# Kernel optimization log

Measured on AMD Instinct MI355X. Metric: run time of the kernel, lower is better.

The kernel has to match this reference:

```python
import jax, jax.numpy as jnp
import numpy as np

DIM = 2048
H = 16
QLR = 1536
KVLR = 512
NOPE = 128
ROPE = 64
VH = 128
QKH = NOPE + ROPE  # 192
B, S = 2, 2048
EPS = 1e-6


def _rmsnorm(x, w):
    return x * jax.lax.rsqrt(jnp.mean(x * x, axis=-1, keepdims=True) + EPS) * w


def _rope_cos_sin(seq_len, r, dtype):
    inv_freq = 1.0 / (10000.0 ** (jnp.arange(0, r, 2, dtype=jnp.float32) / r))
    ang = jnp.arange(seq_len, dtype=jnp.float32)[:, None] * inv_freq  # [S, r/2]
    return jnp.cos(ang).astype(dtype), jnp.sin(ang).astype(dtype)


def _rot(t, cos, sin):
    # rotate-half RoPE on last dim; cos/sin pre-broadcast to t's rank
    t1, t2 = jnp.split(t, 2, axis=-1)
    return jnp.concatenate([t1 * cos - t2 * sin, t2 * cos + t1 * sin], axis=-1)


def setup_inputs() -> dict:
    key = jax.random.key(0)
    ks = jax.random.split(key, 12)
    sd = 0.02
    return {
        "x": jax.random.normal(ks[0], (B, S, DIM), jnp.float32),
        "wqd": jax.random.normal(ks[1], (DIM, QLR), jnp.float32) * sd,
        "bqd": jnp.zeros((QLR,), jnp.float32),
        "qnorm_w": jnp.ones((QLR,), jnp.float32),
        "wqu": jax.random.normal(ks[2], (QLR, H * QKH), jnp.float32) * sd,
        "bqu": jnp.zeros((H * QKH,), jnp.float32),
        "wkvd": jax.random.normal(ks[3], (DIM, KVLR + ROPE), jnp.float32) * sd,
        "bkvd": jnp.zeros((KVLR + ROPE,), jnp.float32),
        "kvnorm_w": jnp.ones((KVLR,), jnp.float32),
        "wkvu": jax.random.normal(ks[4], (KVLR, H * (NOPE + VH)), jnp.float32) * sd,
        "bkvu": jnp.zeros((H * (NOPE + VH),), jnp.float32),
        "wout": jax.random.normal(ks[5], (H * VH, DIM), jnp.float32) * sd,
        "bout": jnp.zeros((DIM,), jnp.float32),
    }


def reference(x, wqd, bqd, qnorm_w, wqu, bqu, wkvd, bkvd, kvnorm_w, wkvu, bkvu, wout, bout):
    b, s, _ = x.shape
    # Q path: low-rank down, RMSNorm, up; split nope / rope
    q = _rmsnorm(x @ wqd + bqd, qnorm_w) @ wqu + bqu        # [b,s,H*QKH]
    q = q.reshape(b, s, H, QKH)
    q_nope, q_rope = q[..., :NOPE], q[..., NOPE:]
    # KV path: joint down-proj -> kv latent + shared rope key
    kvd = x @ wkvd + bkvd                                   # [b,s,KVLR+ROPE]
    kv_lora, k_rope = kvd[..., :KVLR], kvd[..., KVLR:]
    cos, sin = _rope_cos_sin(s, ROPE, x.dtype)
    q_rope = _rot(q_rope, cos[None, :, None, :], sin[None, :, None, :])
    k_rope = _rot(k_rope, cos[None, :, :], sin[None, :, :])  # [b,s,ROPE]
    kvu = _rmsnorm(kv_lora, kvnorm_w) @ wkvu + bkvu          # [b,s,H*(NOPE+VH)]
    kvu = kvu.reshape(b, s, H, NOPE + VH)
    k_nope, v = kvu[..., :NOPE], kvu[..., NOPE:]
    k_rope_b = jnp.broadcast_to(k_rope[:, :, None, :], (b, s, H, ROPE))
    qf = jnp.concatenate([q_nope, q_rope], axis=-1)          # [b,s,H,QKH]
    kf = jnp.concatenate([k_nope, k_rope_b], axis=-1)        # [b,s,H,QKH]
    scale = QKH ** -0.5
    scores = jnp.einsum('bqhd,bkhd->bhqk', qf, kf) * scale
    causal = jnp.tril(jnp.ones((s, s), bool))
    scores = jnp.where(causal, scores, jnp.finfo(scores.dtype).min)
    attn = jax.nn.softmax(scores, axis=-1)
    o = jnp.einsum('bhqk,bkhd->bqhd', attn, v).reshape(b, s, H * VH)
    return o @ wout + bout
```

## Files before the change

### kernel.cpp

```cpp
#include <hip/hip_runtime.h>
#include <hip/hip_bf16.h>
#include <math.h>

#define HH 16
#define SS 2048
#define BBATCH 2
#define NROWS 4096

typedef __attribute__((ext_vector_type(8))) __bf16 bf16x8;
typedef __attribute__((ext_vector_type(4))) float f32x4;
typedef const __attribute__((address_space(1))) unsigned int* gas1_t;
typedef __attribute__((address_space(3))) unsigned int* las3_t;

__device__ __forceinline__ unsigned short f2bf(float f) {
  unsigned u = __builtin_bit_cast(unsigned, f);
  u += 0x7fffu + ((u >> 16) & 1u);
  return (unsigned short)(u >> 16);
}
__device__ __forceinline__ float bf2f(unsigned short u) {
  return __builtin_bit_cast(float, (unsigned)u << 16);
}

__device__ __forceinline__ void gload16(const void* g, void* l) {
  __builtin_amdgcn_global_load_lds((gas1_t)g, (las3_t)l, 16, 0, 0);
}
__device__ __forceinline__ f32x4 mfma16(bf16x8 a, bf16x8 b, f32x4 c) {
  return __builtin_amdgcn_mfma_f32_16x16x32_bf16(a, b, c, 0, 0, 0);
}

__device__ __forceinline__ void transpose_body(const float* __restrict__ W,
                                               unsigned short* __restrict__ Wt,
                                               int K, int N, int Npad,
                                               int bx, int by, float (*tile)[33], int tid) {
  int n0 = bx * 32, k0 = by * 32;
  int tx = tid & 31, ty = tid >> 5;
  for (int i = ty; i < 32; i += 8) {
    int k = k0 + i, n = n0 + tx;
    tile[i][tx] = (k < K && n < N) ? W[(long)k * N + n] : 0.f;
  }
  __syncthreads();
  for (int i = ty; i < 32; i += 8) {
    int n = n0 + i, k = k0 + tx;
    if (n < Npad && k < K) Wt[(long)n * K + k] = f2bf(tile[tx][i]);
  }
}

__global__ __launch_bounds__(256) void k_prep(const float* __restrict__ x,
                                              unsigned short* __restrict__ xb,
                                              const float* __restrict__ wqd,
                                              const float* __restrict__ wqu,
                                              const float* __restrict__ wkvd,
                                              const float* __restrict__ wkvu,
                                              const float* __restrict__ wout,
                                              unsigned short* __restrict__ wqkt,
                                              unsigned short* __restrict__ wqut,
                                              unsigned short* __restrict__ wkvut,
                                              unsigned short* __restrict__ woutt,
                                              const float* __restrict__ bqd,
                                              const float* __restrict__ bkvd,
                                              float* __restrict__ mbias,
                                              float2* __restrict__ rtab) {
  __shared__ float tile[32][33];
  int blk = blockIdx.x;
  int tid = threadIdx.x;
  if (blk < 2048) {
    long n4 = (long)NROWS * 2048 / 4;
    for (long i = (long)blk * 256 + tid; i < n4; i += 2048 * 256) {
      float4 v = ((const float4*)x)[i];
      ushort4 o = { f2bf(v.x), f2bf(v.y), f2bf(v.z), f2bf(v.w) };
      ((ushort4*)xb)[i] = o;
    }
  } else if (blk < 5120) {
    int t = blk - 2048;
    transpose_body(wqd, wqkt, 2048, 1536, 1536, t % 48, t / 48, tile, tid);
  } else if (blk < 9728) {
    int t = blk - 5120;
    transpose_body(wqu, wqut, 1536, 3072, 3072, t % 96, t / 96, tile, tid);
  } else if (blk < 11008) {
    int t = blk - 9728;
    transpose_body(wkvd, wqkt + (size_t)1536 * 2048, 2048, 576, 640, t % 20, t / 20, tile, tid);
  } else if (blk < 13056) {
    int t = blk - 11008;
    transpose_body(wkvu, wkvut, 512, 4096, 4096, t % 128, t / 128, tile, tid);
  } else if (blk < 17152) {
    int t = blk - 13056;
    transpose_body(wout, woutt, 2048, 2048, 2048, t % 64, t / 64, tile, tid);
  } else if (blk < 17161) {
    int i = (blk - 17152) * 256 + tid;
    if (i < 2176) mbias[i] = i < 1536 ? bqd[i] : (i < 2112 ? bkvd[i - 1536] : 0.f);
  } else {
    int t = blk - 17161;
    int s = t * 8 + (tid >> 5);
    int i = tid & 31;
    float inv = powf(10000.f, -(float)i / 32.f);
    float ang = (float)s * inv;
    float sn, cs;
    sincosf(ang, &sn, &cs);
    rtab[s * 32 + i] = make_float2(cs, sn);
  }
}

__global__ __launch_bounds__(256) void k_gemm(const unsigned short* __restrict__ A,
                                              const unsigned short* __restrict__ Bt,
                                              const float* __restrict__ bias,
                                              float* __restrict__ C,
                                              int M, int N, int K) {
  __shared__ unsigned short lA[128 * 32];
  __shared__ unsigned short lB[128 * 32];
  int tid = threadIdx.x;
  int wave = tid >> 6, lane = tid & 63;
  int l15 = lane & 15, lhi = lane >> 4;
  int ntn = (N + 127) >> 7;
  int tm = blockIdx.x / ntn, tn = blockIdx.x % ntn;
  long row0 = (long)tm * 128, col0 = (long)tn * 128;
  int wr = wave >> 1, wc = wave & 1;

  const unsigned short* gA = A + (row0 + (tid >> 2)) * K + (tid & 3) * 8;
  const unsigned short* gB = Bt + (col0 + (tid >> 2)) * K + (tid & 3) * 8;
  unsigned short* lA0 = &lA[tid * 8];
  unsigned short* lB0 = &lB[tid * 8];

  f32x4 acc[4][4] = {};
  for (int k0 = 0; k0 < K; k0 += 32) {
    __syncthreads();
    gload16(gA + k0, lA0);
    gload16(gA + (long)64 * K + k0, lA0 + 2048);
    gload16(gB + k0, lB0);
    gload16(gB + (long)64 * K + k0, lB0 + 2048);
    asm volatile("s_waitcnt vmcnt(0)" ::: "memory");
    __syncthreads();
    bf16x8 af[4], bfr[4];
#pragma unroll
    for (int i = 0; i < 4; ++i) {
      af[i]  = *(const bf16x8*)&lA[(wr * 64 + i * 16 + l15) * 32 + lhi * 8];
      bfr[i] = *(const bf16x8*)&lB[(wc * 64 + i * 16 + l15) * 32 + lhi * 8];
    }
#pragma unroll
    for (int i = 0; i < 4; ++i)
#pragma unroll
      for (int j = 0; j < 4; ++j)
        acc[i][j] = mfma16(af[i], bfr[j], acc[i][j]);
  }
#pragma unroll
  for (int i = 0; i < 4; ++i)
#pragma unroll
    for (int j = 0; j < 4; ++j) {
      long r = row0 + wr * 64 + i * 16 + lhi * 4;
      long c = col0 + wc * 64 + j * 16 + l15;
      if (c < N) {
        float bv = bias[c];
#pragma unroll
        for (int rr = 0; rr < 4; ++rr)
          C[(r + rr) * N + c] = acc[i][j][rr] + bv;
      }
    }
}

__global__ __launch_bounds__(256) void k_gemm_c16(const unsigned short* __restrict__ A,
                                                  const unsigned short* __restrict__ Bt,
                                                  const float* __restrict__ bias,
                                                  unsigned short* __restrict__ C,
                                                  int M, int N, int K) {
  __shared__ unsigned short lA[128 * 32];
  __shared__ unsigned short lB[128 * 32];
  int tid = threadIdx.x;
  int wave = tid >> 6, lane = tid & 63;
  int l15 = lane & 15, lhi = lane >> 4;
  int ntn = (N + 127) >> 7;
  int tm = blockIdx.x / ntn, tn = blockIdx.x % ntn;
  long row0 = (long)tm * 128, col0 = (long)tn * 128;
  int wr = wave >> 1, wc = wave & 1;

  const unsigned short* gA = A + (row0 + (tid >> 2)) * K + (tid & 3) * 8;
  const unsigned short* gB = Bt + (col0 + (tid >> 2)) * K + (tid & 3) * 8;
  unsigned short* lA0 = &lA[tid * 8];
  unsigned short* lB0 = &lB[tid * 8];

  f32x4 acc[4][4] = {};
  for (int k0 = 0; k0 < K; k0 += 32) {
    __syncthreads();
    gload16(gA + k0, lA0);
    gload16(gA + (long)64 * K + k0, lA0 + 2048);
    gload16(gB + k0, lB0);
    gload16(gB + (long)64 * K + k0, lB0 + 2048);
    asm volatile("s_waitcnt vmcnt(0)" ::: "memory");
    __syncthreads();
    bf16x8 af[4], bfr[4];
#pragma unroll
    for (int i = 0; i < 4; ++i) {
      af[i]  = *(const bf16x8*)&lA[(wr * 64 + i * 16 + l15) * 32 + lhi * 8];
      bfr[i] = *(const bf16x8*)&lB[(wc * 64 + i * 16 + l15) * 32 + lhi * 8];
    }
#pragma unroll
    for (int i = 0; i < 4; ++i)
#pragma unroll
      for (int j = 0; j < 4; ++j)
        acc[i][j] = mfma16(af[i], bfr[j], acc[i][j]);
  }
#pragma unroll
  for (int i = 0; i < 4; ++i)
#pragma unroll
    for (int j = 0; j < 4; ++j) {
      long r = row0 + wr * 64 + i * 16 + lhi * 4;
      long c = col0 + wc * 64 + j * 16 + l15;
      if (c < N) {
        float bv = bias[c];
#pragma unroll
        for (int rr = 0; rr < 4; ++rr)
          C[(r + rr) * N + c] = f2bf(acc[i][j][rr] + bv);
      }
    }
}

__global__ __launch_bounds__(256) void k_up(const unsigned short* __restrict__ qn,
                                            const unsigned short* __restrict__ wqut,
                                            const float* __restrict__ bqu,
                                            const unsigned short* __restrict__ kvn,
                                            const unsigned short* __restrict__ wkvut,
                                            const float* __restrict__ bkvu,
                                            const unsigned short* __restrict__ sCb,
                                            const float2* __restrict__ rtab,
                                            unsigned short* __restrict__ qf,
                                            unsigned short* __restrict__ kf3,
                                            unsigned short* __restrict__ vt3) {
  __shared__ unsigned short smem[16384];
  unsigned short* lA = smem;
  unsigned short* lB = smem + 4096;
  int blk = blockIdx.x;
  int tid = threadIdx.x;
  int wave = tid >> 6, lane = tid & 63;
  int l15 = lane & 15, lhi = lane >> 4;
  int wr = wave >> 1, wc = wave & 1;

  if (blk < 768) {
    const int N = 3072, K = 1536;
    int tm = blk / 24, tn = blk % 24;
    long row0 = (long)tm * 128, col0 = (long)tn * 128;
    const unsigned short* gA = qn + (row0 + (tid >> 2)) * K + (tid & 3) * 8;
    const unsigned short* gB = wqut + (col0 + (tid >> 2)) * K + (tid & 3) * 8;
    unsigned short* lA0 = &lA[tid * 8];
    unsigned short* lB0 = &lB[tid * 8];
    f32x4 acc[4][4] = {};
    for (int k0 = 0; k0 < K; k0 += 32) {
      __syncthreads();
      gload16(gA + k0, lA0);
      gload16(gA + (long)64 * K + k0, lA0 + 2048);
      gload16(gB + k0, lB0);
      gload16(gB + (long)64 * K + k0, lB0 + 2048);
      asm volatile("s_waitcnt vmcnt(0)" ::: "memory");
      __syncthreads();
      bf16x8 af[4], bfr[4];
#pragma unroll
      for (int i = 0; i < 4; ++i) {
        af[i]  = *(const bf16x8*)&lA[(wr * 64 + i * 16 + l15) * 32 + lhi * 8];
        bfr[i] = *(const bf16x8*)&lB[(wc * 64 + i * 16 + l15) * 32 + lhi * 8];
      }
#pragma unroll
      for (int i = 0; i < 4; ++i)
#pragma unroll
        for (int j = 0; j < 4; ++j)
          acc[i][j] = mfma16(af[i], bfr[j], acc[i][j]);
    }
    const float scq = 0.07216878364870322f * 1.4426950408889634f;
    int base = (int)col0 + wc * 64;
    int h = base / 192;
    int m192 = base - h * 192;
    float bv[4];
#pragma unroll
    for (int j = 0; j < 4; ++j) bv[j] = bqu[base + j * 16 + l15];
#pragma unroll
    for (int i = 0; i < 4; ++i) {
#pragma unroll
      for (int rr = 0; rr < 4; ++rr) {
        long r = row0 + wr * 64 + i * 16 + lhi * 4 + rr;
        int s = (int)(r & 2047), b = (int)(r >> 11);
        unsigned short* dst = qf + (((long)(b * HH + h)) * SS + s) * 192;
        if (m192 < 128) {
#pragma unroll
          for (int j = 0; j < 4; ++j)
            dst[m192 + j * 16 + l15] = f2bf((acc[i][j][rr] + bv[j]) * scq);
        } else {
#pragma unroll
          for (int j = 0; j < 2; ++j) {
            int ifq = j * 16 + l15;
            float2 cs = rtab[s * 32 + ifq];
            float v1 = acc[i][j][rr] + bv[j];
            float v2 = acc[i][j + 2][rr] + bv[j + 2];
            dst[128 + ifq] = f2bf((v1 * cs.x - v2 * cs.y) * scq);
            dst[160 + ifq] = f2bf((v2 * cs.x + v1 * cs.y) * scq);
          }
        }
      }
    }
  } else if (blk < 1792) {
    const int N = 4096, K = 512;
    int b2 = blk - 768;
    int tm = b2 / 32, tn = b2 % 32;
    long row0 = (long)tm * 128, col0 = (long)tn * 128;
    const unsigned short* gA = kvn + (row0 + (tid >> 2)) * K + (tid & 3) * 8;
    const unsigned short* gB = wkvut + (col0 + (tid >> 2)) * K + (tid & 3) * 8;
    unsigned short* lA0 = &lA[tid * 8];
    unsigned short* lB0 = &lB[tid * 8];
    f32x4 acc[4][4] = {};
    for (int k0 = 0; k0 < K; k0 += 32) {
      __syncthreads();
      gload16(gA + k0, lA0);
      gload16(gA + (long)64 * K + k0, lA0 + 2048);
      gload16(gB + k0, lB0);
      gload16(gB + (long)64 * K + k0, lB0 + 2048);
      asm volatile("s_waitcnt vmcnt(0)" ::: "memory");
      __syncthreads();
      bf16x8 af[4], bfr[4];
#pragma unroll
      for (int i = 0; i < 4; ++i) {
        af[i]  = *(const bf16x8*)&lA[(wr * 64 + i * 16 + l15) * 32 + lhi * 8];
        bfr[i] = *(const bf16x8*)&lB[(wc * 64 + i * 16 + l15) * 32 + lhi * 8];
      }
#pragma unroll
      for (int i = 0; i < 4; ++i)
#pragma unroll
        for (int j = 0; j < 4; ++j)
          acc[i][j] = mfma16(af[i], bfr[j], acc[i][j]);
    }
    int base = (int)col0 + wc * 64;
    int h = base >> 8;
    bool isv = (base & 255) >= 128;
    float bv[4];
#pragma unroll
    for (int j = 0; j < 4; ++j) bv[j] = bkvu[base + j * 16 + l15];
    int b = (int)(row0 >> 11);
    long bh = (long)b * HH + h;
    int lrb = wr * 64;
    __syncthreads();
    if (isv) {
#pragma unroll
      for (int i = 0; i < 4; ++i) {
        int lr = lrb + i * 16 + lhi * 4;
#pragma unroll
        for (int j = 0; j < 4; ++j) {
          int lc = wc * 64 + j * 16 + l15;
          ushort4 pk = { f2bf(acc[i][j][0] + bv[j]), f2bf(acc[i][j][1] + bv[j]),
                         f2bf(acc[i][j][2] + bv[j]), f2bf(acc[i][j][3] + bv[j]) };
          *(ushort4*)&smem[((lr >> 5) << 12) + lc * 32 + (lr & 31)] = pk;
        }
      }
      __syncthreads();
      long dst0 = (bh * 64 + ((row0 & 2047) >> 5)) * 4096;
#pragma unroll
      for (int p = 0; p < 8; ++p) {
        int e = p * 256 + tid;
        *(uint4*)&vt3[dst0 + e * 8] = *(uint4*)&smem[e * 8];
      }
    } else {
#pragma unroll
      for (int i = 0; i < 4; ++i) {
        int lr0 = lrb + i * 16 + lhi * 4;
#pragma unroll
        for (int j = 0; j < 4; ++j) {
          int c = (base & 255) + j * 16 + l15;
          int tbase = ((lr0 >> 4) << 11) + ((c >> 5) << 9) + (((c >> 3) & 3) << 7) + (c & 7);
#pragma unroll
          for (int rr = 0; rr < 4; ++rr)
            smem[tbase + ((lr0 + rr) & 15) * 8] = f2bf(acc[i][j][rr] + bv[j]);
        }
      }
      __syncthreads();
      long kb3 = (bh * 128 + ((row0 & 2047) >> 4)) * 3072;
#pragma unroll
      for (int p = 0; p < 8; ++p) {
        int e = p * 256 + tid;
        int tile = e >> 6;
        int off = (e & 63) * 8;
        long dst = kb3 + ((long)(tile >> 2) * 6 + (tile & 3)) * 512 + off;
        *(uint4*)&kf3[dst] = *(uint4*)&smem[tile * 512 + off];
      }
    }
  } else {
    int t = blk - 1792;
    int bs = t * 4 + (tid >> 6);
    int s = bs & (SS - 1), b = bs >> 11;
    const unsigned short* src = sCb + (long)bs * 2176 + 2048;
    int i = lane & 31;
    float2 cs = rtab[s * 32 + i];
    float t1 = bf2f(src[i]), t2 = bf2f(src[32 + i]);
    float v = (lane < 32) ? (t1 * cs.x - t2 * cs.y) : (t2 * cs.x + t1 * cs.y);
    unsigned short bv = f2bf(v);
    int d = 128 + lane;
    long inner = (long)(d >> 5) * 512 + ((d >> 3) & 3) * 128 + (s & 15) * 8 + (d & 7);
#pragma unroll
    for (int h = 0; h < HH; ++h) {
      long kblk = ((long)(b * HH + h) * 128 + (s >> 4)) * 6;
      kf3[kblk * 512 + inner] = bv;
    }
  }
}

__global__ __launch_bounds__(256) void k_rmsnorm2(const unsigned short* __restrict__ sC,
                                                  const float* __restrict__ qnw,
                                                  const float* __restrict__ kvnw,
                                                  unsigned short* __restrict__ qn,
                                                  unsigned short* __restrict__ kvn) {
  int blk = blockIdx.x;
  long row;
  const unsigned short* x;
  const float* w;
  unsigned short* y;
  int L;
  if (blk < NROWS) {
    row = blk; x = sC + row * 2176; w = qnw; y = qn + row * 1536; L = 1536;
  } else {
    row = blk - NROWS; x = sC + row * 2176 + 1536; w = kvnw; y = kvn + row * 512; L = 512;
  }
  float ss = 0.f;
  int n4 = L >> 2;
  for (int i = threadIdx.x; i < n4; i += 256) {
    ushort4 v = ((const ushort4*)x)[i];
    float a = bf2f(v.x), bb = bf2f(v.y), c = bf2f(v.z), d = bf2f(v.w);
    ss += a * a + bb * bb + c * c + d * d;
  }
  for (int off = 32; off > 0; off >>= 1) ss += __shfl_xor(ss, off);
  __shared__ float sb[4];
  if ((threadIdx.x & 63) == 0) sb[threadIdx.x >> 6] = ss;
  __syncthreads();
  float scale = rsqrtf((sb[0] + sb[1] + sb[2] + sb[3]) / (float)L + 1e-6f);
  for (int i = threadIdx.x; i < L; i += 256)
    y[i] = f2bf(bf2f(x[i]) * scale * w[i]);
}

__global__ __launch_bounds__(256, 4) void k_attn(const unsigned short* __restrict__ qf,
                                                 const unsigned short* __restrict__ kf3,
                                                 const unsigned short* __restrict__ vt3,
                                                 unsigned short* __restrict__ o,
                                                 float* __restrict__ pO,
                                                 float* __restrict__ pml) {
  __shared__ unsigned short kbuf[64 * 192];
  __shared__ unsigned short pbuf[4][16 * 72];
  int tid = threadIdx.x;
  int wave = tid >> 6, lane = tid & 63;
  int l15 = lane & 15, lhi = lane >> 4;
  int idx = blockIdx.x;
  int rp = idx >> 5, bh = idx & 31;
  int qt, part, np;
  if (rp < 32)      { qt = 24 + (rp >> 2); part = rp & 3; np = 4; }
  else if (rp < 56) { int r = rp - 32; qt = 16 + r / 3; part = r % 3; np = 3; }
  else if (rp < 72) { int r = rp - 56; qt = 8 + (r >> 1); part = r & 1; np = 2; }
  else              { qt = 79 - rp; part = 0; np = 1; }
  int nt = qt + 1;
  int t0 = nt * part / np, t1 = nt * (part + 1) / np;
  bool dodiag = (part == np - 1);
  int item;
  if (np == 1) item = -1;
  else {
    int base = (qt < 16) ? (qt - 8) * 2 : (qt < 24) ? 16 + (qt - 16) * 3 : 40 + (qt - 24) * 4;
    item = bh * 72 + base + part;
  }
  int b = bh >> 4, h = bh & 15;
  int q0 = qt * 64;
  const char* kbase = (const char*)(kf3 + (long)bh * 128 * 3072);
  const unsigned short* vfrag0 = vt3 + (long)bh * 64 * 4096 + l15 * 32 + lhi * 8;
  const unsigned short* kread = kbuf + lane * 8;
  unsigned psel = 0x07060302u;

  {
    const char* src = kbase + (long)t0 * 24576 + tid * 16;
    char* dst = (char*)kbuf + tid * 16;
#pragma unroll
    for (int p = 0; p < 6; ++p) gload16(src + p * 4096, dst + p * 4096);
  }

  const unsigned short* Qb = qf + ((long)bh * SS + q0 + wave * 16 + l15) * 192 + lhi * 8;
  bf16x8 qfr[6];
#pragma unroll
  for (int ks = 0; ks < 6; ++ks) qfr[ks] = *(const bf16x8*)(Qb + ks * 32);

  float m = -3e38f, ls = 0.f;
  f32x4 acc[8] = {};
  int qin = wave * 16 + l15;

  for (int t = t0; t < t1; ++t) {
    asm volatile("s_waitcnt vmcnt(0)" ::: "memory");
    __builtin_amdgcn_s_barrier();
    __builtin_amdgcn_sched_barrier(0);

    f32x4 sc[4] = {};
    __builtin_amdgcn_s_setprio(1);
#pragma unroll
    for (int ks = 0; ks < 6; ++ks) {
      bf16x8 kfr[4];
#pragma unroll
      for (int nf = 0; nf < 4; ++nf)
        kfr[nf] = *(const bf16x8*)&kread[(nf * 6 + ks) * 512];
#pragma unroll
      for (int nf = 0; nf < 4; ++nf)
        sc[nf] = mfma16(kfr[nf], qfr[ks], sc[nf]);
    }
    __builtin_amdgcn_s_setprio(0);
    __builtin_amdgcn_sched_barrier(0);
    __builtin_amdgcn_s_barrier();
    __builtin_amdgcn_sched_barrier(0);

    const unsigned short* vtb = vfrag0 + (long)t * 8192;
    bf16x8 v0[8];
#pragma unroll
    for (int nf = 0; nf < 8; ++nf) v0[nf] = *(const bf16x8*)(vtb + nf * 512);
    __builtin_amdgcn_sched_barrier(0);

    if (t + 1 < t1) {
      const char* src = kbase + (long)(t + 1) * 24576 + tid * 16;
      char* dst = (char*)kbuf + tid * 16;
#pragma unroll
      for (int p = 0; p < 6; ++p) gload16(src + p * 4096, dst + p * 4096);
    }

    bool diag = dodiag && (t == t1 - 1);
    float mnf[4];
#pragma unroll
    for (int nf = 0; nf < 4; ++nf) {
      if (diag) {
#pragma unroll
        for (int jj = 0; jj < 4; ++jj) {
          int kin = nf * 16 + lhi * 4 + jj;
          if (kin > qin) sc[nf][jj] = -3e38f;
        }
      }
      mnf[nf] = fmaxf(fmaxf(sc[nf][0], sc[nf][1]), fmaxf(sc[nf][2], sc[nf][3]));
    }
    float mx = fmaxf(fmaxf(mnf[0], mnf[1]), fmaxf(mnf[2], mnf[3]));
    mx = fmaxf(mx, __shfl_xor(mx, 16));
    mx = fmaxf(mx, __shfl_xor(mx, 32));
    if (!__all(mx <= m + 8.f)) {
      float mn = fmaxf(m, mx);
      float alpha = exp2f(m - mn);
      m = mn;
      ls *= alpha;
#pragma unroll
      for (int nf = 0; nf < 8; ++nf)
#pragma unroll
        for (int jj = 0; jj < 4; ++jj) acc[nf][jj] *= alpha;
    }
    float pnf[4];
#pragma unroll
    for (int nf = 0; nf < 4; ++nf) {
      float e0 = exp2f(sc[nf][0] - m), e1 = exp2f(sc[nf][1] - m);
      float e2 = exp2f(sc[nf][2] - m), e3 = exp2f(sc[nf][3] - m);
      pnf[nf] = (e0 + e1) + (e2 + e3);
      unsigned lo, hi;
      asm("v_perm_b32 %0, %1, %2, %3" : "=v"(lo) : "v"(e1), "v"(e0), "s"(psel));
      asm("v_perm_b32 %0, %1, %2, %3" : "=v"(hi) : "v"(e3), "v"(e2), "s"(psel));
      uint2 pk = { lo, hi };
      *(uint2*)&pbuf[wave][l15 * 72 + nf * 16 + lhi * 4] = pk;
    }
    float ps = (pnf[0] + pnf[1]) + (pnf[2] + pnf[3]);
    ps += __shfl_xor(ps, 16);
    ps += __shfl_xor(ps, 32);
    ls += ps;

    {
      bf16x8 pf = *(const bf16x8*)&pbuf[wave][l15 * 72 + lhi * 8];
      __builtin_amdgcn_s_setprio(1);
#pragma unroll
      for (int nf = 0; nf < 8; ++nf) acc[nf] = mfma16(v0[nf], pf, acc[nf]);
      __builtin_amdgcn_s_setprio(0);
    }
    bf16x8 v1[8];
#pragma unroll
    for (int nf = 0; nf < 8; ++nf) v1[nf] = *(const bf16x8*)(vtb + 4096 + nf * 512);
    {
      bf16x8 pf = *(const bf16x8*)&pbuf[wave][l15 * 72 + 32 + lhi * 8];
      __builtin_amdgcn_s_setprio(1);
#pragma unroll
      for (int nf = 0; nf < 8; ++nf) acc[nf] = mfma16(v1[nf], pf, acc[nf]);
      __builtin_amdgcn_s_setprio(0);
    }
  }

  int qloc = wave * 16 + l15;
  if (item < 0) {
    float invl = 1.f / ls;
    long orow = (long)b * SS + q0 + qloc;
#pragma unroll
    for (int nf = 0; nf < 8; ++nf) {
      ushort4 ov = { f2bf(acc[nf][0] * invl), f2bf(acc[nf][1] * invl),
                     f2bf(acc[nf][2] * invl), f2bf(acc[nf][3] * invl) };
      *(ushort4*)&o[orow * 2048 + h * 128 + nf * 16 + lhi * 4] = ov;
    }
  } else {
    float* po = pO + (long)item * 8192 + qloc * 128;
#pragma unroll
    for (int nf = 0; nf < 8; ++nf)
      *(float4*)&po[nf * 16 + lhi * 4] = __builtin_bit_cast(float4, acc[nf]);
    if (lhi == 0) {
      pml[(long)item * 128 + qloc * 2] = m;
      pml[(long)item * 128 + qloc * 2 + 1] = ls;
    }
  }
}

__global__ __launch_bounds__(256) void k_merge(const float* __restrict__ pO,
                                               const float* __restrict__ pml,
                                               unsigned short* __restrict__ o) {
  int g = blockIdx.x;
  int bh = g / 24, qt = (g % 24) + 8;
  int b = bh >> 4, h = bh & 15;
  int q0 = qt * 64;
  int np = qt < 16 ? 2 : (qt < 24 ? 3 : 4);
  int base = (qt < 16) ? (qt - 8) * 2 : (qt < 24) ? 16 + (qt - 16) * 3 : 40 + (qt - 24) * 4;
  long i0 = (long)bh * 72 + base;
  __shared__ float wts[4][64];
  int tid = threadIdx.x;
  if (tid < 64) {
    float mp0 = -3e38f, mp1 = -3e38f, mp2 = -3e38f, mp3 = -3e38f;
    float lp0 = 0.f, lp1 = 0.f, lp2 = 0.f, lp3 = 0.f;
    mp0 = pml[(i0 + 0) * 128 + tid * 2]; lp0 = pml[(i0 + 0) * 128 + tid * 2 + 1];
    mp1 = pml[(i0 + 1) * 128 + tid * 2]; lp1 = pml[(i0 + 1) * 128 + tid * 2 + 1];
    if (np > 2) { mp2 = pml[(i0 + 2) * 128 + tid * 2]; lp2 = pml[(i0 + 2) * 128 + tid * 2 + 1]; }
    if (np > 3) { mp3 = pml[(i0 + 3) * 128 + tid * 2]; lp3 = pml[(i0 + 3) * 128 + tid * 2 + 1]; }
    float mm = fmaxf(fmaxf(mp0, mp1), fmaxf(mp2, mp3));
    float w0 = exp2f(mp0 - mm), w1 = exp2f(mp1 - mm);
    float w2 = (np > 2) ? exp2f(mp2 - mm) : 0.f;
    float w3 = (np > 3) ? exp2f(mp3 - mm) : 0.f;
    float inv = 1.f / (lp0 * w0 + lp1 * w1 + lp2 * w2 + lp3 * w3);
    wts[0][tid] = w0 * inv; wts[1][tid] = w1 * inv;
    wts[2][tid] = w2 * inv; wts[3][tid] = w3 * inv;
  }
  __syncthreads();
#pragma unroll
  for (int pp = 0; pp < 8; ++pp) {
    int e = pp * 256 + tid;
    int q = e >> 5, d4 = (e & 31) * 4;
    float4 s = { 0.f, 0.f, 0.f, 0.f };
#pragma unroll
    for (int p = 0; p < 4; ++p) {
      if (p < np) {
        float4 a = *(const float4*)&pO[(i0 + p) * 8192 + q * 128 + d4];
        float w = wts[p][q];
        s.x += a.x * w; s.y += a.y * w; s.z += a.z * w; s.w += a.w * w;
      }
    }
    ushort4 ov = { f2bf(s.x), f2bf(s.y), f2bf(s.z), f2bf(s.w) };
    *(ushort4*)&o[((long)b * SS + q0 + q) * 2048 + h * 128 + d4] = ov;
  }
}

extern "C" void kernel_launch(void* const* d_in, const int* in_sizes, int n_in,
                              void* d_out, int out_size, void* d_ws, size_t ws_size,
                              hipStream_t stream) {
  const float* x    = (const float*)d_in[0];
  const float* wqd  = (const float*)d_in[1];
  const float* bqd  = (const float*)d_in[2];
  const float* qnw  = (const float*)d_in[3];
  const float* wqu  = (const float*)d_in[4];
  const float* bqu  = (const float*)d_in[5];
  const float* wkvd = (const float*)d_in[6];
  const float* bkvd = (const float*)d_in[7];
  const float* kvnw = (const float*)d_in[8];
  const float* wkvu = (const float*)d_in[9];
  const float* bkvu = (const float*)d_in[10];
  const float* wout = (const float*)d_in[11];
  const float* bout = (const float*)d_in[12];
  float* out = (float*)d_out;

  char* ws = (char*)d_ws;
  size_t off = 0;
  auto alloc = [&](size_t sz) {
    char* p = ws + off;
    off += (sz + 255) & ~(size_t)255;
    return p;
  };
  unsigned short* xb    = (unsigned short*)alloc((size_t)NROWS * 2048 * 2);
  unsigned short* wqkt  = (unsigned short*)alloc((size_t)2176 * 2048 * 2);
  unsigned short* wqut  = (unsigned short*)alloc((size_t)3072 * 1536 * 2);
  unsigned short* wkvut = (unsigned short*)alloc((size_t)4096 * 512 * 2);
  unsigned short* woutt = (unsigned short*)alloc((size_t)2048 * 2048 * 2);
  unsigned short* qn    = (unsigned short*)alloc((size_t)NROWS * 1536 * 2);
  unsigned short* kvn   = (unsigned short*)alloc((size_t)NROWS * 512 * 2);
  unsigned short* qfb   = (unsigned short*)alloc((size_t)32 * SS * 192 * 2);
  unsigned short* kfb   = (unsigned short*)alloc((size_t)32 * SS * 192 * 2);
  unsigned short* vtb   = (unsigned short*)alloc((size_t)32 * 128 * SS * 2);
  unsigned short* ob    = (unsigned short*)alloc((size_t)NROWS * 2048 * 2);
  float*  mbias = (float*)alloc((size_t)2176 * 4);
  float2* rtab  = (float2*)alloc((size_t)SS * 32 * 8);
  float*  pO    = (float*)alloc((size_t)2304 * 8192 * 4);
  float*  pml   = (float*)alloc((size_t)2304 * 128 * 4);
  unsigned short* sCb = (unsigned short*)alloc((size_t)NROWS * 2176 * 2);

  k_prep<<<17417, 256, 0, stream>>>(x, xb, wqd, wqu, wkvd, wkvu, wout,
                                    wqkt, wqut, wkvut, woutt, bqd, bkvd, mbias, rtab);

  k_gemm_c16<<<32 * 17, 256, 0, stream>>>(xb, wqkt, mbias, sCb, NROWS, 2176, 2048);

  k_rmsnorm2<<<2 * NROWS, 256, 0, stream>>>(sCb, qnw, kvnw, qn, kvn);

  k_up<<<2816, 256, 0, stream>>>(qn, wqut, bqu, kvn, wkvut, bkvu, sCb, rtab,
                                 qfb, kfb, vtb);

  k_attn<<<2560, 256, 0, stream>>>(qfb, kfb, vtb, ob, pO, pml);
  k_merge<<<768, 256, 0, stream>>>(pO, pml, ob);

  k_gemm<<<32 * 16, 256, 0, stream>>>(ob, woutt, bout, out, NROWS, 2048, 2048);
}
```

Measured before the change: 391.7 us.

## Use K=64 XOR-swizzled GEMM core and store attention partials in bf16

Introduces a shared GEMM mainloop that stages 64-wide K slices into LDS with an XOR swizzle. This halves the number of barrier/wait rounds and avoids LDS bank conflicts on fragment reads, and it is applied to all four GEMM sites. Separately, split-KV attention partial outputs are written as bf16 instead of fp32, which halves the partial-buffer traffic between the attention and merge kernels. The cost is double the LDS per block, which may reduce occupancy, plus a small precision loss in the partials.

```diff
diff --git a/kernel.cpp b/kernel.cpp
--- a/kernel.cpp
+++ b/kernel.cpp
@@ -26,6 +26,47 @@
 }
 __device__ __forceinline__ f32x4 mfma16(bf16x8 a, bf16x8 b, f32x4 c) {
   return __builtin_amdgcn_mfma_f32_16x16x32_bf16(a, b, c, 0, 0, 0);
+}
+
+__device__ __forceinline__ void gemm_core64(const unsigned short* __restrict__ A,
+                                            const unsigned short* __restrict__ Bt,
+                                            int K, long row0, long col0, int tid,
+                                            unsigned short* lA, unsigned short* lB,
+                                            f32x4 (*acc)[4]) {
+  int wave = tid >> 6, lane = tid & 63;
+  int l15 = lane & 15, lhi = lane >> 4;
+  int wr = wave >> 1, wc = wave & 1;
+  int trow = tid >> 3, tcg = tid & 7;
+  const unsigned short* gA = A + (row0 + trow) * K + ((tcg ^ (trow & 7)) * 8);
+  const unsigned short* gB = Bt + (col0 + trow) * K + ((tcg ^ (trow & 7)) * 8);
+  unsigned short* lA0 = &lA[tid * 8];
+  unsigned short* lB0 = &lB[tid * 8];
+  for (int k0 = 0; k0 < K; k0 += 64) {
+    __syncthreads();
+#pragma unroll
+    for (int p = 0; p < 4; ++p) {
+      gload16(gA + (long)p * 32 * K + k0, lA0 + p * 2048);
+      gload16(gB + (long)p * 32 * K + k0, lB0 + p * 2048);
+    }
+    asm volatile("s_waitcnt vmcnt(0)" ::: "memory");
+    __syncthreads();
+#pragma unroll
+    for (int kk = 0; kk < 2; ++kk) {
+      bf16x8 af[4], bfr[4];
+#pragma unroll
+      for (int i = 0; i < 4; ++i) {
+        int rA = wr * 64 + i * 16 + l15;
+        int rB = wc * 64 + i * 16 + l15;
+        af[i]  = *(const bf16x8*)&lA[rA * 64 + (((kk * 4 + lhi) ^ (rA & 7)) * 8)];
+        bfr[i] = *(const bf16x8*)&lB[rB * 64 + (((kk * 4 + lhi) ^ (rB & 7)) * 8)];
+      }
+#pragma unroll
+      for (int i = 0; i < 4; ++i)
+#pragma unroll
+        for (int j = 0; j < 4; ++j)
+          acc[i][j] = mfma16(af[i], bfr[j], acc[i][j]);
+    }
+  }
 }
 
 __device__ __forceinline__ void transpose_body(const float* __restrict__ W,
@@ -105,8 +146,8 @@
                                               const float* __restrict__ bias,
                                               float* __restrict__ C,
                                               int M, int N, int K) {
-  __shared__ unsigned short lA[128 * 32];
-  __shared__ unsigned short lB[128 * 32];
+  __shared__ unsigned short lA[128 * 64];
+  __shared__ unsigned short lB[128 * 64];
   int tid = threadIdx.x;
   int wave = tid >> 6, lane = tid & 63;
   int l15 = lane & 15, lhi = lane >> 4;
@@ -115,32 +156,9 @@
   long row0 = (long)tm * 128, col0 = (long)tn * 128;
   int wr = wave >> 1, wc = wave & 1;
 
-  const unsigned short* gA = A + (row0 + (tid >> 2)) * K + (tid & 3) * 8;
-  const unsigned short* gB = Bt + (col0 + (tid >> 2)) * K + (tid & 3) * 8;
-  unsigned short* lA0 = &lA[tid * 8];
-  unsigned short* lB0 = &lB[tid * 8];
-
   f32x4 acc[4][4] = {};
-  for (int k0 = 0; k0 < K; k0 += 32) {
-    __syncthreads();
-    gload16(gA + k0, lA0);
-    gload16(gA + (long)64 * K + k0, lA0 + 2048);
-    gload16(gB + k0, lB0);
-    gload16(gB + (long)64 * K + k0, lB0 + 2048);
-    asm volatile("s_waitcnt vmcnt(0)" ::: "memory");
-    __syncthreads();
-    bf16x8 af[4], bfr[4];
-#pragma unroll
-    for (int i = 0; i < 4; ++i) {
-      af[i]  = *(const bf16x8*)&lA[(wr * 64 + i * 16 + l15) * 32 + lhi * 8];
-      bfr[i] = *(const bf16x8*)&lB[(wc * 64 + i * 16 + l15) * 32 + lhi * 8];
-    }
-#pragma unroll
-    for (int i = 0; i < 4; ++i)
-#pragma unroll
-      for (int j = 0; j < 4; ++j)
-        acc[i][j] = mfma16(af[i], bfr[j], acc[i][j]);
-  }
+  gemm_core64(A, Bt, K, row0, col0, tid, lA, lB, acc);
+
 #pragma unroll
   for (int i = 0; i < 4; ++i)
 #pragma unroll
@@ -161,8 +179,8 @@
                                                   const float* __restrict__ bias,
                                                   unsigned short* __restrict__ C,
                                                   int M, int N, int K) {
-  __shared__ unsigned short lA[128 * 32];
-  __shared__ unsigned short lB[128 * 32];
+  __shared__ unsigned short lA[128 * 64];
+  __shared__ unsigned short lB[128 * 64];
   int tid = threadIdx.x;
   int wave = tid >> 6, lane = tid & 63;
   int l15 = lane & 15, lhi = lane >> 4;
@@ -171,32 +189,9 @@
   long row0 = (long)tm * 128, col0 = (long)tn * 128;
   int wr = wave >> 1, wc = wave & 1;
 
-  const unsigned short* gA = A + (row0 + (tid >> 2)) * K + (tid & 3) * 8;
-  const unsigned short* gB = Bt + (col0 + (tid >> 2)) * K + (tid & 3) * 8;
-  unsigned short* lA0 = &lA[tid * 8];
-  unsigned short* lB0 = &lB[tid * 8];
-
   f32x4 acc[4][4] = {};
-  for (int k0 = 0; k0 < K; k0 += 32) {
-    __syncthreads();
-    gload16(gA + k0, lA0);
-    gload16(gA + (long)64 * K + k0, lA0 + 2048);
-    gload16(gB + k0, lB0);
-    gload16(gB + (long)64 * K + k0, lB0 + 2048);
-    asm volatile("s_waitcnt vmcnt(0)" ::: "memory");
-    __syncthreads();
-    bf16x8 af[4], bfr[4];
-#pragma unroll
-    for (int i = 0; i < 4; ++i) {
-      af[i]  = *(const bf16x8*)&lA[(wr * 64 + i * 16 + l15) * 32 + lhi * 8];
-      bfr[i] = *(const bf16x8*)&lB[(wc * 64 + i * 16 + l15) * 32 + lhi * 8];
-    }
-#pragma unroll
-    for (int i = 0; i < 4; ++i)
-#pragma unroll
-      for (int j = 0; j < 4; ++j)
-        acc[i][j] = mfma16(af[i], bfr[j], acc[i][j]);
-  }
+  gemm_core64(A, Bt, K, row0, col0, tid, lA, lB, acc);
+
 #pragma unroll
   for (int i = 0; i < 4; ++i)
 #pragma unroll
@@ -225,7 +220,7 @@
                                             unsigned short* __restrict__ vt3) {
   __shared__ unsigned short smem[16384];
   unsigned short* lA = smem;
-  unsigned short* lB = smem + 4096;
+  unsigned short* lB = smem + 8192;
   int blk = blockIdx.x;
   int tid = threadIdx.x;
   int wave = tid >> 6, lane = tid & 63;
@@ -233,34 +228,12 @@
   int wr = wave >> 1, wc = wave & 1;
 
   if (blk < 768) {
-    const int N = 3072, K = 1536;
+    const int K = 1536;
     int tm = blk / 24, tn = blk % 24;
     long row0 = (long)tm * 128, col0 = (long)tn * 128;
-    const unsigned short* gA = qn + (row0 + (tid >> 2)) * K + (tid & 3) * 8;
-    const unsigned short* gB = wqut + (col0 + (tid >> 2)) * K + (tid & 3) * 8;
-    unsigned short* lA0 = &lA[tid * 8];
-    unsigned short* lB0 = &lB[tid * 8];
     f32x4 acc[4][4] = {};
-    for (int k0 = 0; k0 < K; k0 += 32) {
-      __syncthreads();
-      gload16(gA + k0, lA0);
-      gload16(gA + (long)64 * K + k0, lA0 + 2048);
-      gload16(gB + k0, lB0);
-      gload16(gB + (long)64 * K + k0, lB0 + 2048);
-      asm volatile("s_waitcnt vmcnt(0)" ::: "memory");
-      __syncthreads();
-      bf16x8 af[4], bfr[4];
-#pragma unroll
-      for (int i = 0; i < 4; ++i) {
-        af[i]  = *(const bf16x8*)&lA[(wr * 64 + i * 16 + l15) * 32 + lhi * 8];
-        bfr[i] = *(const bf16x8*)&lB[(wc * 64 + i * 16 + l15) * 32 + lhi * 8];
-      }
-#pragma unroll
-      for (int i = 0; i < 4; ++i)
-#pragma unroll
-        for (int j = 0; j < 4; ++j)
-          acc[i][j] = mfma16(af[i], bfr[j], acc[i][j]);
-    }
+    gemm_core64(qn, wqut, K, row0, col0, tid, lA, lB, acc);
+
     const float scq = 0.07216878364870322f * 1.4426950408889634f;
     int base = (int)col0 + wc * 64;
     int h = base / 192;
@@ -293,35 +266,13 @@
       }
     }
   } else if (blk < 1792) {
-    const int N = 4096, K = 512;
+    const int K = 512;
     int b2 = blk - 768;
     int tm = b2 / 32, tn = b2 % 32;
     long row0 = (long)tm * 128, col0 = (long)tn * 128;
-    const unsigned short* gA = kvn + (row0 + (tid >> 2)) * K + (tid & 3) * 8;
-    const unsigned short* gB = wkvut + (col0 + (tid >> 2)) * K + (tid & 3) * 8;
-    unsigned short* lA0 = &lA[tid * 8];
-    unsigned short* lB0 = &lB[tid * 8];
     f32x4 acc[4][4] = {};
-    for (int k0 = 0; k0 < K; k0 += 32) {
-      __syncthreads();
-      gload16(gA + k0, lA0);
-      gload16(gA + (long)64 * K + k0, lA0 + 2048);
-      gload16(gB + k0, lB0);
-      gload16(gB + (long)64 * K + k0, lB0 + 2048);
-      asm volatile("s_waitcnt vmcnt(0)" ::: "memory");
-      __syncthreads();
-      bf16x8 af[4], bfr[4];
-#pragma unroll
-      for (int i = 0; i < 4; ++i) {
-        af[i]  = *(const bf16x8*)&lA[(wr * 64 + i * 16 + l15) * 32 + lhi * 8];
-        bfr[i] = *(const bf16x8*)&lB[(wc * 64 + i * 16 + l15) * 32 + lhi * 8];
-      }
-#pragma unroll
-      for (int i = 0; i < 4; ++i)
-#pragma unroll
-        for (int j = 0; j < 4; ++j)
-          acc[i][j] = mfma16(af[i], bfr[j], acc[i][j]);
-    }
+    gemm_core64(kvn, wkvut, K, row0, col0, tid, lA, lB, acc);
+
     int base = (int)col0 + wc * 64;
     int h = base >> 8;
     bool isv = (base & 255) >= 128;
@@ -431,7 +382,7 @@
                                                  const unsigned short* __restrict__ kf3,
                                                  const unsigned short* __restrict__ vt3,
                                                  unsigned short* __restrict__ o,
-                                                 float* __restrict__ pO,
+                                                 unsigned short* __restrict__ pOb,
                                                  float* __restrict__ pml) {
   __shared__ unsigned short kbuf[64 * 192];
   __shared__ unsigned short pbuf[4][16 * 72];
@@ -585,10 +536,13 @@
       *(ushort4*)&o[orow * 2048 + h * 128 + nf * 16 + lhi * 4] = ov;
     }
   } else {
-    float* po = pO + (long)item * 8192 + qloc * 128;
-#pragma unroll
-    for (int nf = 0; nf < 8; ++nf)
-      *(float4*)&po[nf * 16 + lhi * 4] = __builtin_bit_cast(float4, acc[nf]);
+    unsigned short* po = pOb + (long)item * 8192 + qloc * 128;
+#pragma unroll
+    for (int nf = 0; nf < 8; ++nf) {
+      ushort4 pv = { f2bf(acc[nf][0]), f2bf(acc[nf][1]),
+                     f2bf(acc[nf][2]), f2bf(acc[nf][3]) };
+      *(ushort4*)&po[nf * 16 + lhi * 4] = pv;
+    }
     if (lhi == 0) {
       pml[(long)item * 128 + qloc * 2] = m;
       pml[(long)item * 128 + qloc * 2 + 1] = ls;
@@ -596,7 +550,7 @@
   }
 }
 
-__global__ __launch_bounds__(256) void k_merge(const float* __restrict__ pO,
+__global__ __launch_bounds__(256) void k_merge(const unsigned short* __restrict__ pOb,
                                                const float* __restrict__ pml,
                                                unsigned short* __restrict__ o) {
   int g = blockIdx.x;
@@ -625,20 +579,30 @@
   }
   __syncthreads();
 #pragma unroll
-  for (int pp = 0; pp < 8; ++pp) {
+  for (int pp = 0; pp < 4; ++pp) {
     int e = pp * 256 + tid;
-    int q = e >> 5, d4 = (e & 31) * 4;
-    float4 s = { 0.f, 0.f, 0.f, 0.f };
+    int q = e >> 4, d8 = (e & 15) * 8;
+    float s[8] = {};
 #pragma unroll
     for (int p = 0; p < 4; ++p) {
       if (p < np) {
-        float4 a = *(const float4*)&pO[(i0 + p) * 8192 + q * 128 + d4];
+        uint4 v = *(const uint4*)&pOb[(i0 + p) * 8192 + q * 128 + d8];
         float w = wts[p][q];
-        s.x += a.x * w; s.y += a.y * w; s.z += a.z * w; s.w += a.w * w;
-      }
-    }
-    ushort4 ov = { f2bf(s.x), f2bf(s.y), f2bf(s.z), f2bf(s.w) };
-    *(ushort4*)&o[((long)b * SS + q0 + q) * 2048 + h * 128 + d4] = ov;
+        s[0] += bf2f((unsigned short)(v.x & 0xffff)) * w;
+        s[1] += bf2f((unsigned short)(v.x >> 16)) * w;
+        s[2] += bf2f((unsigned short)(v.y & 0xffff)) * w;
+        s[3] += bf2f((unsigned short)(v.y >> 16)) * w;
+        s[4] += bf2f((unsigned short)(v.z & 0xffff)) * w;
+        s[5] += bf2f((unsigned short)(v.z >> 16)) * w;
+        s[6] += bf2f((unsigned short)(v.w & 0xffff)) * w;
+        s[7] += bf2f((unsigned short)(v.w >> 16)) * w;
+      }
+    }
+    long ob_ = ((long)b * SS + q0 + q) * 2048 + h * 128 + d8;
+    ushort4 o0 = { f2bf(s[0]), f2bf(s[1]), f2bf(s[2]), f2bf(s[3]) };
+    ushort4 o1 = { f2bf(s[4]), f2bf(s[5]), f2bf(s[6]), f2bf(s[7]) };
+    *(ushort4*)&o[ob_] = o0;
+    *(ushort4*)&o[ob_ + 4] = o1;
   }
 }
 
@@ -680,7 +644,7 @@
   unsigned short* ob    = (unsigned short*)alloc((size_t)NROWS * 2048 * 2);
   float*  mbias = (float*)alloc((size_t)2176 * 4);
   float2* rtab  = (float2*)alloc((size_t)SS * 32 * 8);
-  float*  pO    = (float*)alloc((size_t)2304 * 8192 * 4);
+  unsigned short* pOb = (unsigned short*)alloc((size_t)2304 * 8192 * 2);
   float*  pml   = (float*)alloc((size_t)2304 * 128 * 4);
   unsigned short* sCb = (unsigned short*)alloc((size_t)NROWS * 2176 * 2);
 
@@ -694,8 +658,8 @@
   k_up<<<2816, 256, 0, stream>>>(qn, wqut, bqu, kvn, wkvut, bkvu, sCb, rtab,
                                  qfb, kfb, vtb);
 
-  k_attn<<<2560, 256, 0, stream>>>(qfb, kfb, vtb, ob, pO, pml);
-  k_merge<<<768, 256, 0, stream>>>(pO, pml, ob);
+  k_attn<<<2560, 256, 0, stream>>>(qfb, kfb, vtb, ob, pOb, pml);
+  k_merge<<<768, 256, 0, stream>>>(pOb, pml, ob);
 
   k_gemm<<<32 * 16, 256, 0, stream>>>(ob, woutt, bout, out, NROWS, 2048, 2048);
 }
```

New measurement: 346.0 us. 1.13x faster.
